# Performance work log

Measured on AMD Instinct MI355X. Metric: run time of the kernel, lower is better.

## Reference

```python
import jax, jax.numpy as jnp
import numpy as np

B, N, DIN, DOUT = 8, 2048, 512, 256
NUM_BUCKETS = 20


def setup_inputs() -> dict:
    key = jax.random.key(0)
    ks = jax.random.split(key, 12)
    s_in = 1.0 / np.sqrt(DIN)
    s_out = 1.0 / np.sqrt(DOUT)
    return {
        "x": jax.random.normal(ks[0], (B, N, DIN), dtype=jnp.float32),
        "price_rank": jax.random.randint(ks[1], (B, N), 0, N, dtype=jnp.int64),
        "Wq": jax.random.uniform(ks[2], (DOUT, DIN), jnp.float32, -s_in, s_in),
        "bq": jax.random.uniform(ks[3], (DOUT,), jnp.float32, -s_in, s_in),
        "Wk": jax.random.uniform(ks[4], (DOUT, DIN), jnp.float32, -s_in, s_in),
        "bk": jax.random.uniform(ks[5], (DOUT,), jnp.float32, -s_in, s_in),
        "Wv": jax.random.uniform(ks[6], (DOUT, DIN), jnp.float32, -s_in, s_in),
        "bv": jax.random.uniform(ks[7], (DOUT,), jnp.float32, -s_in, s_in),
        "Ws": jax.random.uniform(ks[8], (1, DOUT), jnp.float32, -s_out, s_out),
        "bs": jax.random.uniform(ks[9], (1,), jnp.float32, -s_out, s_out),
        "rank_emb": jax.random.normal(ks[10], (NUM_BUCKETS, 1), dtype=jnp.float32),
        "rank_w": jnp.ones((1,), dtype=jnp.float32),
    }


def reference(x, price_rank, Wq, bq, Wk, bk, Wv, bv, Ws, bs, rank_emb, rank_w):
    scale = jnp.sqrt(jnp.asarray(DOUT, dtype=x.dtype))
    q = jnp.einsum("bnd,od->bno", x, Wq) + bq  # [B,N,DOUT]
    k = jnp.einsum("bnd,od->bno", x, Wk) + bk
    v = jnp.einsum("bnd,od->bno", x, Wv) + bv
    scores = jnp.einsum("bno,bmo->bnm", q, k) / scale  # [B,N,N]
    # learned pairwise rank-distance bias gate
    rank_dist = jnp.abs(price_rank[:, :, None] - price_rank[:, None, :])
    buckets = jnp.clip(rank_dist // 5, 0, NUM_BUCKETS - 1)  # [B,N,N] int
    prior = rank_emb[buckets, 0]  # gather embedding, squeeze last dim
    gate = jax.nn.sigmoid(rank_w[0] * prior)
    scores = scores * gate
    attn = jax.nn.softmax(scores, axis=2)
    context = jnp.einsum("bnm,bmo->bno", attn, v)  # [B,N,DOUT]
    winner = jax.nn.sigmoid(jnp.einsum("bno,uo->bnu", context, Ws) + bs)[..., 0]
    return winner  # [B,N]
```

## Files before the change

kernel.cpp:

```cpp
#include <hip/hip_runtime.h>
#include <hip/hip_bf16.h>

#define B_    8
#define N_    2048
#define DIN_  512
#define DOUT_ 256
#define NBUCK 20

typedef __attribute__((ext_vector_type(8))) short  short8;
typedef __attribute__((ext_vector_type(4))) float  floatx4;

__device__ __forceinline__ unsigned short f2b(float f) {
    __hip_bfloat16 h = __float2bfloat16(f);
    unsigned short u;
    __builtin_memcpy(&u, &h, 2);
    return u;
}

__device__ __forceinline__ void load_lds16(const unsigned short* g, unsigned short* l) {
    __builtin_amdgcn_global_load_lds(
        (const __attribute__((address_space(1))) unsigned int*)g,
        (__attribute__((address_space(3))) unsigned int*)l, 16, 0, 0);
}

__device__ __forceinline__ float fexp2(float x) {
    float r;
    asm("v_exp_f32 %0, %1" : "=v"(r) : "v"(x));
    return r;
}

__global__ __launch_bounds__(256) void prep_kernel(
    const float* __restrict__ Wv, const float* __restrict__ Ws,
    const float* __restrict__ bv,
    float* __restrict__ wvs, float* __restrict__ bvs) {
    const int blk = blockIdx.x, tid = threadIdx.x;
    __shared__ float wsl[DOUT_];
    wsl[tid] = Ws[tid];
    __syncthreads();
    if (tid < 128) {
        int d = blk * 128 + tid;
        float s0 = 0.f, s1 = 0.f, s2 = 0.f, s3 = 0.f;
#pragma unroll 8
        for (int o = 0; o < DOUT_; o += 4) {
            s0 += Wv[(size_t)(o + 0) * DIN_ + d] * wsl[o + 0];
            s1 += Wv[(size_t)(o + 1) * DIN_ + d] * wsl[o + 1];
            s2 += Wv[(size_t)(o + 2) * DIN_ + d] * wsl[o + 2];
            s3 += Wv[(size_t)(o + 3) * DIN_ + d] * wsl[o + 3];
        }
        wvs[d] = (s0 + s1) + (s2 + s3);
    }
    if (blk == 0 && tid < 64) {
        float bb = wsl[tid] * bv[tid] + wsl[tid + 64] * bv[tid + 64] +
                   wsl[tid + 128] * bv[tid + 128] + wsl[tid + 192] * bv[tid + 192];
        for (int off = 1; off < 64; off <<= 1) bb += __shfl_xor(bb, off, 64);
        if (tid == 0) *bvs = bb;
    }
}

__global__ __launch_bounds__(256) void cvt_x_kernel(const float* __restrict__ x,
                                                    const float* __restrict__ wvs,
                                                    const float* __restrict__ bvs,
                                                    const float* __restrict__ wq,
                                                    const float* __restrict__ wk,
                                                    unsigned short* __restrict__ xb,
                                                    unsigned short* __restrict__ wdst,
                                                    float* __restrict__ vw) {
    int tid = threadIdx.x;
    if (blockIdx.x >= 4096) {
        int i = ((blockIdx.x - 4096) * 256 + tid) * 8;
        const float* src = (i < 131072) ? (wq + i) : (wk + (i - 131072));
        float4 a = *(const float4*)(src);
        float4 b = *(const float4*)(src + 4);
        uint4 r;
        r.x = f2b(a.x) | ((unsigned)f2b(a.y) << 16);
        r.y = f2b(a.z) | ((unsigned)f2b(a.w) << 16);
        r.z = f2b(b.x) | ((unsigned)f2b(b.y) << 16);
        r.w = f2b(b.z) | ((unsigned)f2b(b.w) << 16);
        *(uint4*)(wdst + i) = r;
        return;
    }
    int wave = tid >> 6, lane = tid & 63;
    int row = blockIdx.x * 4 + wave;
    size_t base = (size_t)row * DIN_ + lane * 8;
    float4 a = *(const float4*)(x + base);
    float4 b = *(const float4*)(x + base + 4);
    float4 wa = *(const float4*)(wvs + lane * 8);
    float4 wb = *(const float4*)(wvs + lane * 8 + 4);
    uint4 r;
    r.x = f2b(a.x) | ((unsigned)f2b(a.y) << 16);
    r.y = f2b(a.z) | ((unsigned)f2b(a.w) << 16);
    r.z = f2b(b.x) | ((unsigned)f2b(b.y) << 16);
    r.w = f2b(b.z) | ((unsigned)f2b(b.w) << 16);
    *(uint4*)(xb + base) = r;
    float d = a.x * wa.x + a.y * wa.y + a.z * wa.z + a.w * wa.w +
              b.x * wb.x + b.y * wb.y + b.z * wb.z + b.w * wb.w;
    for (int off = 1; off < 64; off <<= 1) d += __shfl_xor(d, off, 64);
    if (lane == 0) vw[row] = d + *bvs;
}

__global__ __launch_bounds__(256, 2) void qkv_kernel(
    const unsigned short* __restrict__ xb, const unsigned short* __restrict__ wb,
    const float* __restrict__ bq, const float* __restrict__ bk,
    unsigned short* __restrict__ qo, unsigned short* __restrict__ ko) {
    __shared__ unsigned short alds[2][128 * 64];
    __shared__ unsigned short blds[2][128 * 64];
    const int g = blockIdx.x;
    const int xcd = g & 7, t2 = g >> 3;
    const int colBlk = t2 & 3, rowGrp = t2 >> 2;
    const int rowBlk = rowGrp * 8 + xcd;
    const int tid = threadIdx.x;
    const int wave = tid >> 6, lane = tid & 63, quad = lane >> 4, l16 = lane & 15;
    const int wr = wave >> 1, wc = wave & 1;
    const int row0 = rowBlk * 128, col0 = colBlk * 128;
    const int sw3 = l16 & 7;

    floatx4 acc[4][4];
#pragma unroll
    for (int i = 0; i < 4; ++i)
#pragma unroll
        for (int j = 0; j < 4; ++j) acc[i][j] = (floatx4){0.f, 0.f, 0.f, 0.f};

    const int gseg = (lane & 7) ^ (lane >> 3);
    const unsigned short* ag = xb + (size_t)(row0 + wave * 8 + (lane >> 3)) * DIN_ + gseg * 8;
    const unsigned short* bg = wb + (size_t)(col0 + wave * 8 + (lane >> 3)) * DIN_ + gseg * 8;

#pragma unroll
    for (int i = 0; i < 4; ++i) {
        load_lds16(ag + (size_t)i * 32 * DIN_, &alds[0][wave * 512 + i * 2048]);
        load_lds16(bg + (size_t)i * 32 * DIN_, &blds[0][wave * 512 + i * 2048]);
    }
    __syncthreads();

#pragma unroll 1
    for (int t = 0; t < 8; ++t) {
        const unsigned short* al = (t & 1) ? alds[1] : alds[0];
        const unsigned short* bl = (t & 1) ? blds[1] : blds[0];
        unsigned short* aln = (t & 1) ? &alds[0][0] : &alds[1][0];
        unsigned short* bln = (t & 1) ? &blds[0][0] : &blds[1][0];
        if (t < 7) {
            size_t koff = (size_t)(t + 1) * 64;
#pragma unroll
            for (int i = 0; i < 4; ++i) {
                load_lds16(ag + (size_t)i * 32 * DIN_ + koff, aln + wave * 512 + i * 2048);
                load_lds16(bg + (size_t)i * 32 * DIN_ + koff, bln + wave * 512 + i * 2048);
            }
        }
#pragma unroll
        for (int h = 0; h < 2; ++h) {
            short8 af[4], bf[4];
#pragma unroll
            for (int f = 0; f < 4; ++f) {
                int ar = wr * 64 + f * 16 + l16;
                int br = wc * 64 + f * 16 + l16;
                int s  = (h * 4 + quad) ^ sw3;
                af[f] = *(const short8*)&al[(size_t)ar * 64 + s * 8];
                bf[f] = *(const short8*)&bl[(size_t)br * 64 + s * 8];
            }
#pragma unroll
            for (int i = 0; i < 4; ++i)
#pragma unroll
                for (int j = 0; j < 4; ++j)
                    acc[i][j] = __builtin_amdgcn_mfma_f32_16x16x32_bf16(af[i], bf[j], acc[i][j], 0, 0, 0);
        }
        __syncthreads();
    }

#pragma unroll
    for (int j = 0; j < 4; ++j) {
        int col = col0 + wc * 64 + j * 16 + l16;
        unsigned short* dst = (col < 256) ? qo : ko;
        float bias = (col < 256) ? bq[col] : bk[col - 256];
        int c = col & 255;
#pragma unroll
        for (int i = 0; i < 4; ++i)
#pragma unroll
            for (int r = 0; r < 4; ++r) {
                int row = row0 + wr * 64 + i * 16 + quad * 4 + r;
                dst[(size_t)row * DOUT_ + c] = f2b(acc[i][j][r] + bias);
            }
    }
}

__global__ __launch_bounds__(512, 2) void attn_kernel(
    const unsigned short* __restrict__ q, const unsigned short* __restrict__ k,
    const float* __restrict__ vw, const int* __restrict__ pr,
    const float* __restrict__ rank_emb, const float* __restrict__ rank_w,
    const float* __restrict__ bs, float* __restrict__ out) {
    const int g = blockIdx.x;
    const int b = g & 7, rblk = g >> 3;
    const int tid = threadIdx.x, wave = tid >> 6, lane = tid & 63;
    const int quad = lane >> 4, l16 = lane & 15;
    const int n0 = rblk * 64;
    const int rg = wave >> 2, ch = wave & 3;

    __shared__ unsigned short kbuf[2][32768];
    __shared__ float gtab_r[NBUCK * 32];
    __shared__ float lL[8][32], wdL[8][32];

    for (int t = tid; t < NBUCK * 32; t += 512)
        gtab_r[t] = 0.0625f * 1.44269504f /
                    (1.f + __expf(-rank_w[0] * rank_emb[t >> 5]));

    const unsigned short* qb = q + (size_t)b * N_ * DOUT_;
    const unsigned short* kb = k + (size_t)b * N_ * DOUT_;
    const float* vwb = vw + b * N_;
    const int* prb = pr + b * N_;
    const int l8 = lane & 7;
    const int l31 = lane & 31;

    short8 qf[2][8];
#pragma unroll
    for (int a = 0; a < 2; ++a)
#pragma unroll
        for (int c = 0; c < 8; ++c)
            qf[a][c] = *(const short8*)(qb + (size_t)(n0 + rg * 32 + a * 16 + l16) * DOUT_ + c * 32 + quad * 8);

    float prn5[2][4];
#pragma unroll
    for (int a = 0; a < 2; ++a)
#pragma unroll
        for (int r = 0; r < 4; ++r)
            prn5[a][r] = (float)prb[n0 + rg * 32 + a * 16 + quad * 4 + r] * 0.2f;

    float lacc[2][4], wacc[2][4];
#pragma unroll
    for (int a = 0; a < 2; ++a)
#pragma unroll
        for (int r = 0; r < 4; ++r) { lacc[a][r] = 0.f; wacc[a][r] = 0.f; }

    const int stg_rbase = wave * 2 + (lane >> 5);
    const int stg_gseg  = (lane & 31) ^ (stg_rbase & 7);
    const unsigned short* stg_src0 = kb + (size_t)stg_rbase * DOUT_ + stg_gseg * 8;
    unsigned short* sdst0 = &kbuf[0][wave * 512];
    unsigned short* sdst1 = &kbuf[1][wave * 512];

    auto stage = [&](int j, unsigned short* sdst) {
        const unsigned short* src = stg_src0 + (size_t)j * 128 * DOUT_;
#pragma unroll
        for (int i = 0; i < 8; ++i)
            load_lds16(src + (size_t)i * 4096, sdst + i * 4096);
    };
    auto mfma = [&](floatx4 (&s)[2][2], const unsigned short* buf) {
#pragma unroll
        for (int a = 0; a < 2; ++a)
#pragma unroll
            for (int cf = 0; cf < 2; ++cf) s[a][cf] = (floatx4){0.f, 0.f, 0.f, 0.f};
        __builtin_amdgcn_s_setprio(1);
#pragma unroll
        for (int c = 0; c < 8; ++c) {
            int seg = (c * 4 + quad) ^ l8;
            short8 kf0 = *(const short8*)&buf[(size_t)(ch * 32 + l16) * 256 + seg * 8];
            short8 kf1 = *(const short8*)&buf[(size_t)(ch * 32 + 16 + l16) * 256 + seg * 8];
            s[0][0] = __builtin_amdgcn_mfma_f32_16x16x32_bf16(qf[0][c], kf0, s[0][0], 0, 0, 0);
            s[1][0] = __builtin_amdgcn_mfma_f32_16x16x32_bf16(qf[1][c], kf0, s[1][0], 0, 0, 0);
            s[0][1] = __builtin_amdgcn_mfma_f32_16x16x32_bf16(qf[0][c], kf1, s[0][1], 0, 0, 0);
            s[1][1] = __builtin_amdgcn_mfma_f32_16x16x32_bf16(qf[1][c], kf1, s[1][1], 0, 0, 0);
        }
        __builtin_amdgcn_s_setprio(0);
    };
    auto gate = [&](floatx4 (&s)[2][2], int pm0, int pm1, float w0, float w1) {
        float pm5_0 = (float)pm0 * 0.2f, pm5_1 = (float)pm1 * 0.2f;
#pragma unroll
        for (int a = 0; a < 2; ++a)
#pragma unroll
            for (int r = 0; r < 4; ++r) {
                float d0 = fabsf(prn5[a][r] - pm5_0);
                int i0 = (int)fminf(d0, 19.0f);
                float p0 = fexp2(s[a][0][r] * gtab_r[i0 * 32 + l31]);
                lacc[a][r] += p0;
                wacc[a][r] += p0 * w0;
                float d1 = fabsf(prn5[a][r] - pm5_1);
                int i1 = (int)fminf(d1, 19.0f);
                float p1 = fexp2(s[a][1][r] * gtab_r[i1 * 32 + l31]);
                lacc[a][r] += p1;
                wacc[a][r] += p1 * w1;
            }
    };

    floatx4 sA[2][2], sB[2][2];
    const int colq = ch * 32 + l16;

    stage(0, sdst0);
    int   pmA0 = prb[colq], pmA1 = prb[colq + 16];
    float wA0 = vwb[colq], wA1 = vwb[colq + 16];
    __syncthreads();
    stage(1, sdst1);
    int   pmB0 = prb[128 + colq], pmB1 = prb[128 + colq + 16];
    float wB0 = vwb[128 + colq], wB1 = vwb[128 + colq + 16];
    mfma(sA, kbuf[0]);
    __syncthreads();

#pragma unroll 1
    for (int jj = 0; jj < 7; ++jj) {
        {
            int jn = 2 * jj + 2;
            stage(jn, sdst0);
            int   p0 = prb[jn * 128 + colq], p1 = prb[jn * 128 + colq + 16];
            float w0 = vwb[jn * 128 + colq], w1 = vwb[jn * 128 + colq + 16];
            mfma(sB, kbuf[1]);
            __builtin_amdgcn_sched_barrier(0);
            gate(sA, pmA0, pmA1, wA0, wA1);
            pmA0 = p0; pmA1 = p1; wA0 = w0; wA1 = w1;
            __syncthreads();
        }
        {
            int jn = 2 * jj + 3;
            stage(jn, sdst1);
            int   p0 = prb[jn * 128 + colq], p1 = prb[jn * 128 + colq + 16];
            float w0 = vwb[jn * 128 + colq], w1 = vwb[jn * 128 + colq + 16];
            mfma(sA, kbuf[0]);
            __builtin_amdgcn_sched_barrier(0);
            gate(sB, pmB0, pmB1, wB0, wB1);
            pmB0 = p0; pmB1 = p1; wB0 = w0; wB1 = w1;
            __syncthreads();
        }
    }
    mfma(sB, kbuf[1]);
    __builtin_amdgcn_sched_barrier(0);
    gate(sA, pmA0, pmA1, wA0, wA1);
    gate(sB, pmB0, pmB1, wB0, wB1);

#pragma unroll
    for (int off = 1; off < 16; off <<= 1) {
#pragma unroll
        for (int a = 0; a < 2; ++a)
#pragma unroll
            for (int r = 0; r < 4; ++r) {
                lacc[a][r] += __shfl_xor(lacc[a][r], off, 64);
                wacc[a][r] += __shfl_xor(wacc[a][r], off, 64);
            }
    }
    if (l16 == 0) {
#pragma unroll
        for (int a = 0; a < 2; ++a)
#pragma unroll
            for (int r = 0; r < 4; ++r) {
                int row = a * 16 + quad * 4 + r;
                lL[wave][row]  = lacc[a][r];
                wdL[wave][row] = wacc[a][r];
            }
    }
    __syncthreads();
    if (tid < 64) {
        int rg2 = tid >> 5, sub = tid & 31;
        float l = 0.f, wd = 0.f;
#pragma unroll
        for (int c2 = 0; c2 < 4; ++c2) {
            l  += lL[rg2 * 4 + c2][sub];
            wd += wdL[rg2 * 4 + c2][sub];
        }
        float logit = wd / l + bs[0];
        out[(size_t)b * N_ + n0 + tid] = 1.f / (1.f + __expf(-logit));
    }
}

extern "C" void kernel_launch(void* const* d_in, const int* in_sizes, int n_in,
                              void* d_out, int out_size, void* d_ws, size_t ws_size,
                              hipStream_t stream) {
    const float* x   = (const float*)d_in[0];
    const int*   pr  = (const int*)d_in[1];
    const float* Wq  = (const float*)d_in[2];
    const float* bq  = (const float*)d_in[3];
    const float* Wk  = (const float*)d_in[4];
    const float* bk  = (const float*)d_in[5];
    const float* Wv  = (const float*)d_in[6];
    const float* bv  = (const float*)d_in[7];
    const float* Ws  = (const float*)d_in[8];
    const float* bs  = (const float*)d_in[9];
    const float* remb = (const float*)d_in[10];
    const float* rw   = (const float*)d_in[11];
    float* out = (float*)d_out;

    char* ws = (char*)d_ws;
    unsigned short* xb  = (unsigned short*)ws;
    unsigned short* wb  = (unsigned short*)(ws + 16777216);
    unsigned short* q   = (unsigned short*)(ws + 17301504);
    unsigned short* kk  = (unsigned short*)(ws + 25690112);
    float*          vwp = (float*)(ws + 34078720);
    float*          wvs = (float*)(ws + 34144256);
    float*          bvs = (float*)(ws + 34146304);

    hipLaunchKernelGGL(prep_kernel, dim3(4), dim3(256), 0, stream,
                       Wv, Ws, bv, wvs, bvs);
    hipLaunchKernelGGL(cvt_x_kernel, dim3(4224), dim3(256), 0, stream,
                       x, wvs, bvs, Wq, Wk, xb, wb, vwp);
    hipLaunchKernelGGL(qkv_kernel, dim3(512), dim3(256), 0, stream,
                       xb, wb, bq, bk, q, kk);
    hipLaunchKernelGGL(attn_kernel, dim3(256), dim3(512), 0, stream,
                       q, kk, vwp, pr, remb, rw, bs, out);
}
```

Baseline: 146.0 us.

## Load K fragments directly from global memory instead of double-buffered LDS staging

Removes the double-buffered LDS staging of K tiles (global_load_lds plus per-step barriers) and has each wave read its K fragments straight from global/L2 inside a simple 16-step loop. This frees 128 KB of shared memory and drops the block-wide syncs that gated each tile. The cost is redundant global reads: the two row-group waves now fetch the same K rows, the reads are strided per lane and not coalesced, and there is no software prefetch to hide load latency behind the MFMA and gate work.

```diff
diff --git a/kernel.cpp b/kernel.cpp
--- a/kernel.cpp
+++ b/kernel.cpp
@@ -193,19 +193,18 @@
     const int n0 = rblk * 64;
     const int rg = wave >> 2, ch = wave & 3;
 
-    __shared__ unsigned short kbuf[2][32768];
     __shared__ float gtab_r[NBUCK * 32];
     __shared__ float lL[8][32], wdL[8][32];
 
     for (int t = tid; t < NBUCK * 32; t += 512)
         gtab_r[t] = 0.0625f * 1.44269504f /
                     (1.f + __expf(-rank_w[0] * rank_emb[t >> 5]));
+    __syncthreads();
 
     const unsigned short* qb = q + (size_t)b * N_ * DOUT_;
     const unsigned short* kb = k + (size_t)b * N_ * DOUT_;
     const float* vwb = vw + b * N_;
     const int* prb = pr + b * N_;
-    const int l8 = lane & 7;
     const int l31 = lane & 31;
 
     short8 qf[2][8];
@@ -228,37 +227,34 @@
 #pragma unroll
         for (int r = 0; r < 4; ++r) { lacc[a][r] = 0.f; wacc[a][r] = 0.f; }
 
-    const int stg_rbase = wave * 2 + (lane >> 5);
-    const int stg_gseg  = (lane & 31) ^ (stg_rbase & 7);
-    const unsigned short* stg_src0 = kb + (size_t)stg_rbase * DOUT_ + stg_gseg * 8;
-    unsigned short* sdst0 = &kbuf[0][wave * 512];
-    unsigned short* sdst1 = &kbuf[1][wave * 512];
-
-    auto stage = [&](int j, unsigned short* sdst) {
-        const unsigned short* src = stg_src0 + (size_t)j * 128 * DOUT_;
-#pragma unroll
-        for (int i = 0; i < 8; ++i)
-            load_lds16(src + (size_t)i * 4096, sdst + i * 4096);
-    };
-    auto mfma = [&](floatx4 (&s)[2][2], const unsigned short* buf) {
-#pragma unroll
-        for (int a = 0; a < 2; ++a)
-#pragma unroll
-            for (int cf = 0; cf < 2; ++cf) s[a][cf] = (floatx4){0.f, 0.f, 0.f, 0.f};
+    const unsigned short* kc0 = kb + (size_t)(ch * 32 + l16) * DOUT_ + quad * 8;
+    const unsigned short* kc1 = kc0 + (size_t)16 * DOUT_;
+    const int colq = ch * 32 + l16;
+
+#pragma unroll 1
+    for (int j = 0; j < 16; ++j) {
+        const size_t jb = (size_t)j * 128 * DOUT_;
+        int   pm0 = prb[j * 128 + colq], pm1 = prb[j * 128 + colq + 16];
+        float w0  = vwb[j * 128 + colq], w1  = vwb[j * 128 + colq + 16];
+
+        floatx4 s0[2], s1[2];
+        s0[0] = (floatx4){0.f, 0.f, 0.f, 0.f}; s0[1] = s0[0];
+        s1[0] = s0[0]; s1[1] = s0[0];
         __builtin_amdgcn_s_setprio(1);
 #pragma unroll
         for (int c = 0; c < 8; ++c) {
-            int seg = (c * 4 + quad) ^ l8;
-            short8 kf0 = *(const short8*)&buf[(size_t)(ch * 32 + l16) * 256 + seg * 8];
-            short8 kf1 = *(const short8*)&buf[(size_t)(ch * 32 + 16 + l16) * 256 + seg * 8];
-            s[0][0] = __builtin_amdgcn_mfma_f32_16x16x32_bf16(qf[0][c], kf0, s[0][0], 0, 0, 0);
-            s[1][0] = __builtin_amdgcn_mfma_f32_16x16x32_bf16(qf[1][c], kf0, s[1][0], 0, 0, 0);
-            s[0][1] = __builtin_amdgcn_mfma_f32_16x16x32_bf16(qf[0][c], kf1, s[0][1], 0, 0, 0);
-            s[1][1] = __builtin_amdgcn_mfma_f32_16x16x32_bf16(qf[1][c], kf1, s[1][1], 0, 0, 0);
+            short8 kf = *(const short8*)(kc0 + jb + c * 32);
+            s0[0] = __builtin_amdgcn_mfma_f32_16x16x32_bf16(qf[0][c], kf, s0[0], 0, 0, 0);
+            s0[1] = __builtin_amdgcn_mfma_f32_16x16x32_bf16(qf[1][c], kf, s0[1], 0, 0, 0);
+        }
+#pragma unroll
+        for (int c = 0; c < 8; ++c) {
+            short8 kf = *(const short8*)(kc1 + jb + c * 32);
+            s1[0] = __builtin_amdgcn_mfma_f32_16x16x32_bf16(qf[0][c], kf, s1[0], 0, 0, 0);
+            s1[1] = __builtin_amdgcn_mfma_f32_16x16x32_bf16(qf[1][c], kf, s1[1], 0, 0, 0);
         }
         __builtin_amdgcn_s_setprio(0);
-    };
-    auto gate = [&](floatx4 (&s)[2][2], int pm0, int pm1, float w0, float w1) {
+
         float pm5_0 = (float)pm0 * 0.2f, pm5_1 = (float)pm1 * 0.2f;
 #pragma unroll
         for (int a = 0; a < 2; ++a)
@@ -266,59 +262,16 @@
             for (int r = 0; r < 4; ++r) {
                 float d0 = fabsf(prn5[a][r] - pm5_0);
                 int i0 = (int)fminf(d0, 19.0f);
-                float p0 = fexp2(s[a][0][r] * gtab_r[i0 * 32 + l31]);
+                float p0 = fexp2(s0[a][r] * gtab_r[i0 * 32 + l31]);
                 lacc[a][r] += p0;
                 wacc[a][r] += p0 * w0;
                 float d1 = fabsf(prn5[a][r] - pm5_1);
                 int i1 = (int)fminf(d1, 19.0f);
-                float p1 = fexp2(s[a][1][r] * gtab_r[i1 * 32 + l31]);
+                float p1 = fexp2(s1[a][r] * gtab_r[i1 * 32 + l31]);
                 lacc[a][r] += p1;
                 wacc[a][r] += p1 * w1;
             }
-    };
-
-    floatx4 sA[2][2], sB[2][2];
-    const int colq = ch * 32 + l16;
-
-    stage(0, sdst0);
-    int   pmA0 = prb[colq], pmA1 = prb[colq + 16];
-    float wA0 = vwb[colq], wA1 = vwb[colq + 16];
-    __syncthreads();
-    stage(1, sdst1);
-    int   pmB0 = prb[128 + colq], pmB1 = prb[128 + colq + 16];
-    float wB0 = vwb[128 + colq], wB1 = vwb[128 + colq + 16];
-    mfma(sA, kbuf[0]);
-    __syncthreads();
-
-#pragma unroll 1
-    for (int jj = 0; jj < 7; ++jj) {
-        {
-            int jn = 2 * jj + 2;
-            stage(jn, sdst0);
-            int   p0 = prb[jn * 128 + colq], p1 = prb[jn * 128 + colq + 16];
-            float w0 = vwb[jn * 128 + colq], w1 = vwb[jn * 128 + colq + 16];
-            mfma(sB, kbuf[1]);
-            __builtin_amdgcn_sched_barrier(0);
-            gate(sA, pmA0, pmA1, wA0, wA1);
-            pmA0 = p0; pmA1 = p1; wA0 = w0; wA1 = w1;
-            __syncthreads();
-        }
-        {
-            int jn = 2 * jj + 3;
-            stage(jn, sdst1);
-            int   p0 = prb[jn * 128 + colq], p1 = prb[jn * 128 + colq + 16];
-            float w0 = vwb[jn * 128 + colq], w1 = vwb[jn * 128 + colq + 16];
-            mfma(sA, kbuf[0]);
-            __builtin_amdgcn_sched_barrier(0);
-            gate(sB, pmB0, pmB1, wB0, wB1);
-            pmB0 = p0; pmB1 = p1; wB0 = w0; wB1 = w1;
-            __syncthreads();
-        }
-    }
-    mfma(sB, kbuf[1]);
-    __builtin_amdgcn_sched_barrier(0);
-    gate(sA, pmA0, pmA1, wA0, wA1);
-    gate(sB, pmB0, pmB1, wB0, wB1);
+    }
 
 #pragma unroll
     for (int off = 1; off < 16; off <<= 1) {
```

Measured after the change: 179.6 us. 1.23x slower.
